# Kernel optimization log

Measured on AMD Instinct MI355X. Metric: run time of the kernel, lower is better.

Reference implementation:

```python
import jax, jax.numpy as jnp
import numpy as np

IN_CHANNELS = 192
BAND_DIM = IN_CHANNELS // 3   # 64
HEADS = 4
HEAD_DIM = BAND_DIM // HEADS  # 16
SCALE = HEAD_DIM ** -0.5


def setup_inputs() -> dict:
    key = jax.random.key(0)
    k1, k2, k3 = jax.random.split(key, 3)
    B, H, W = 8, 128, 128
    hf = jax.random.normal(k1, (B, IN_CHANNELS, H, W), dtype=jnp.float32)
    # torch Linear weights, stored as (in, out) for direct matmul
    W_qkv = jax.random.normal(k2, (BAND_DIM, 3 * BAND_DIM), dtype=jnp.float32) * (BAND_DIM ** -0.5)
    W_proj = jax.random.normal(k3, (BAND_DIM, BAND_DIM), dtype=jnp.float32) * (BAND_DIM ** -0.5)
    b_proj = jnp.zeros((BAND_DIM,), dtype=jnp.float32)
    res_scale = jnp.float32(0.5)
    return {"hf": hf, "W_qkv": W_qkv, "W_proj": W_proj, "b_proj": b_proj, "res_scale": res_scale}


def reference(hf, W_qkv, W_proj, b_proj, res_scale):
    B, Ctot, H, W = hf.shape
    bd, h, hd = BAND_DIM, HEADS, HEAD_DIM
    # (B, 3, bd, H, W) -> (B, H, W, 3, bd) -> (N, 3, bd)
    x = hf.reshape(B, 3, bd, H, W).transpose(0, 3, 4, 1, 2).reshape(-1, 3, bd)
    qkv = x @ W_qkv                                   # (N, 3, 3*bd)
    q, k, v = jnp.split(qkv, 3, axis=-1)
    # (N, 3, bd) -> (N, heads, 3, hd)
    def split_heads(t):
        return t.reshape(-1, 3, h, hd).transpose(0, 2, 1, 3)
    q, k, v = split_heads(q), split_heads(k), split_heads(v)
    attn = jnp.einsum('nhqd,nhkd->nhqk', q, k) * SCALE  # (N, heads, 3, 3)
    attn = jax.nn.softmax(attn, axis=-1)
    y = jnp.einsum('nhqk,nhkd->nhqd', attn, v)          # (N, heads, 3, hd)
    y = y.transpose(0, 2, 1, 3).reshape(-1, 3, bd)      # (N, 3, bd)
    y = y @ W_proj + b_proj
    # (N, 3, bd) -> (B, H, W, 3, bd) -> (B, Ctot, H, W)
    y = y.reshape(B, H, W, 3, bd).transpose(0, 3, 4, 1, 2).reshape(B, Ctot, H, W)
    return hf + res_scale * y
```

## Files before the change

kernel.cpp:

```cpp
#include <hip/hip_runtime.h>


typedef __attribute__((ext_vector_type(8))) short bf16x8;
typedef __attribute__((ext_vector_type(4))) float f32x4;

constexpr int kHW = 16384;
constexpr int kC = 192;

__device__ __forceinline__ unsigned short f2bf(float f) {
  unsigned int u = __float_as_uint(f);
  return (unsigned short)((u + 0x7fffu + ((u >> 16) & 1u)) >> 16);
}

__global__ void pack_weights(const float* __restrict__ Wqkv,
                             const float* __restrict__ Wproj,
                             unsigned char* __restrict__ wsc) {
  const int tid = threadIdx.x;
  const int wid = tid >> 6;
  const int l = tid & 63;
  const int c = l & 15;
  const int g = l >> 4;
  for (int f = wid; f < 24; f += 4) {
    const int m = f >> 1, s = f & 1;
    const int row = m * 16 + c;
    const int k0 = s * 32 + g * 8;
    bf16x8 wf;
#pragma unroll
    for (int j = 0; j < 8; ++j) wf[j] = (short)f2bf(Wqkv[(k0 + j) * 192 + row]);
    *(bf16x8*)(wsc + f * 1024 + l * 16) = wf;
  }
  for (int f = wid; f < 8; f += 4) {
    const int m = f >> 1, s = f & 1;
    const int row = m * 16 + c;
    const int k0 = s * 32 + g * 8;
    bf16x8 wf;
#pragma unroll
    for (int j = 0; j < 8; ++j) wf[j] = (short)f2bf(Wproj[(k0 + j) * 64 + row]);
    *(bf16x8*)(wsc + 24576 + f * 1024 + l * 16) = wf;
  }
}

template <int H>
__device__ __forceinline__ void head_compute(const char* wl, int l,
                                             const bf16x8 (&Xf)[3][2],
                                             uint2 (&pk)[3]) {
  const f32x4 zz = {0.f, 0.f, 0.f, 0.f};
  const bf16x8 qA0 = *(const bf16x8*)(wl + (H * 2 + 0) * 1024 + l * 16);
  const bf16x8 qA1 = *(const bf16x8*)(wl + (H * 2 + 1) * 1024 + l * 16);
  const bf16x8 kA0 = *(const bf16x8*)(wl + ((4 + H) * 2 + 0) * 1024 + l * 16);
  const bf16x8 kA1 = *(const bf16x8*)(wl + ((4 + H) * 2 + 1) * 1024 + l * 16);
  f32x4 q[3], k[3];
#pragma unroll
  for (int b = 0; b < 3; ++b) {
    q[b] = __builtin_amdgcn_mfma_f32_16x16x32_bf16(qA0, Xf[b][0], zz, 0, 0, 0);
    q[b] = __builtin_amdgcn_mfma_f32_16x16x32_bf16(qA1, Xf[b][1], q[b], 0, 0, 0);
    k[b] = __builtin_amdgcn_mfma_f32_16x16x32_bf16(kA0, Xf[b][0], zz, 0, 0, 0);
    k[b] = __builtin_amdgcn_mfma_f32_16x16x32_bf16(kA1, Xf[b][1], k[b], 0, 0, 0);
  }
  float P[3][3];
#pragma unroll
  for (int r1 = 0; r1 < 3; ++r1) {
    float sc[3];
#pragma unroll
    for (int r2 = 0; r2 < 3; ++r2) {
      float d = q[r1][0] * k[r2][0] + q[r1][1] * k[r2][1] +
                q[r1][2] * k[r2][2] + q[r1][3] * k[r2][3];
      d += __shfl_xor(d, 16);
      d += __shfl_xor(d, 32);
      sc[r2] = d * 0.25f;
    }
    const float mx = fmaxf(sc[0], fmaxf(sc[1], sc[2]));
    const float e0 = __expf(sc[0] - mx);
    const float e1 = __expf(sc[1] - mx);
    const float e2 = __expf(sc[2] - mx);
    const float inv = 1.f / (e0 + e1 + e2);
    P[r1][0] = e0 * inv;
    P[r1][1] = e1 * inv;
    P[r1][2] = e2 * inv;
  }
  const bf16x8 vA0 = *(const bf16x8*)(wl + ((8 + H) * 2 + 0) * 1024 + l * 16);
  const bf16x8 vA1 = *(const bf16x8*)(wl + ((8 + H) * 2 + 1) * 1024 + l * 16);
  f32x4 v[3];
#pragma unroll
  for (int b = 0; b < 3; ++b) {
    v[b] = __builtin_amdgcn_mfma_f32_16x16x32_bf16(vA0, Xf[b][0], zz, 0, 0, 0);
    v[b] = __builtin_amdgcn_mfma_f32_16x16x32_bf16(vA1, Xf[b][1], v[b], 0, 0, 0);
  }
#pragma unroll
  for (int r1 = 0; r1 < 3; ++r1) {
    f32x4 y = P[r1][0] * v[0] + P[r1][1] * v[1] + P[r1][2] * v[2];
    uint2 p;
    p.x = (unsigned)f2bf(y[0]) | ((unsigned)f2bf(y[1]) << 16);
    p.y = (unsigned)f2bf(y[2]) | ((unsigned)f2bf(y[3]) << 16);
    pk[r1] = p;
  }
}

__device__ __forceinline__ bf16x8 build_frag(uint2 pkA, uint2 pkB, int srcA,
                                             bool hi) {
  uint2 a0, a1, b0, b1;
  a0.x = (unsigned)__shfl((int)pkA.x, srcA, 64);
  a0.y = (unsigned)__shfl((int)pkA.y, srcA, 64);
  a1.x = (unsigned)__shfl((int)pkB.x, srcA, 64);
  a1.y = (unsigned)__shfl((int)pkB.y, srcA, 64);
  const int srcB = srcA + 16;
  b0.x = (unsigned)__shfl((int)pkA.x, srcB, 64);
  b0.y = (unsigned)__shfl((int)pkA.y, srcB, 64);
  b1.x = (unsigned)__shfl((int)pkB.x, srcB, 64);
  b1.y = (unsigned)__shfl((int)pkB.y, srcB, 64);
  const uint2 lo = hi ? a1 : a0;
  const uint2 hi2 = hi ? b1 : b0;
  union {
    unsigned u[4];
    bf16x8 v;
  } r;
  r.u[0] = lo.x;
  r.u[1] = lo.y;
  r.u[2] = hi2.x;
  r.u[3] = hi2.y;
  return r.v;
}

__global__ __launch_bounds__(256, 4) void hfattn_mfma10(
    const float* __restrict__ hf,
    const unsigned char* __restrict__ wfr,
    const float* __restrict__ bproj,
    const float* __restrict__ rscale,
    float* __restrict__ out) {
  __shared__ char wlds[32768];

  const int tid = threadIdx.x;
  const int wid = tid >> 6;
  const int l = tid & 63;
  const int c = l & 15;
  const int g = l >> 4;

  const f32x4 zz = {0.f, 0.f, 0.f, 0.f};

  const int pxB = blockIdx.x * 64 + wid * 16;
  const int b8 = pxB >> 14;
  const int blkBase = b8 * (kC * kHW);
  const int hw = (pxB & (kHW - 1)) + c;
  const float* __restrict__ hfp = hf + blkBase + hw;
  float* __restrict__ outp = out + blkBase + hw;

  const float rv = rscale[0];

#pragma unroll
  for (int i = 0; i < 8; ++i) {
    __builtin_amdgcn_global_load_lds(
        (const __attribute__((address_space(1))) unsigned int*)(wfr +
                                                                wid * 8192 +
                                                                i * 1024 +
                                                                l * 16),
        (__attribute__((address_space(3))) unsigned int*)(wlds + wid * 8192 +
                                                          i * 1024),
        16, 0, 0);
  }

  float xr[3][2][8];
#pragma unroll
  for (int b = 0; b < 3; ++b)
#pragma unroll
    for (int s = 0; s < 2; ++s)
#pragma unroll
      for (int j = 0; j < 8; ++j)
        xr[b][s][j] = hfp[(b * 64 + s * 32 + g * 8 + j) * kHW];
  __builtin_amdgcn_sched_barrier(0);

  bf16x8 Xf[3][2];
#pragma unroll
  for (int b = 0; b < 3; ++b)
#pragma unroll
    for (int s = 0; s < 2; ++s) {
      bf16x8 xf;
#pragma unroll
      for (int j = 0; j < 8; ++j) xf[j] = (short)f2bf(xr[b][s][j]);
      Xf[b][s] = xf;
    }

  asm volatile("s_waitcnt vmcnt(0)" ::: "memory");
  __syncthreads();

  const int srcA = ((g & 1) * 2) * 16 + c;
  const bool hi = (g >> 1) & 1;

  uint2 pkA[3], pkB[3];
  bf16x8 yS0[3], yS1[3];

  head_compute<0>(wlds, l, Xf, pkA);
  __builtin_amdgcn_sched_barrier(0);
  head_compute<1>(wlds, l, Xf, pkB);
  __builtin_amdgcn_sched_barrier(0);
#pragma unroll
  for (int b = 0; b < 3; ++b) yS0[b] = build_frag(pkA[b], pkB[b], srcA, hi);
  __builtin_amdgcn_sched_barrier(0);
  head_compute<2>(wlds, l, Xf, pkA);
  __builtin_amdgcn_sched_barrier(0);
  head_compute<3>(wlds, l, Xf, pkB);
  __builtin_amdgcn_sched_barrier(0);
#pragma unroll
  for (int b = 0; b < 3; ++b) yS1[b] = build_frag(pkA[b], pkB[b], srcA, hi);

  float bias_[4][4];
#pragma unroll
  for (int m = 0; m < 4; ++m) {
    const float4 bj = *(const float4*)(bproj + m * 16 + g * 4);
    bias_[m][0] = bj.x;
    bias_[m][1] = bj.y;
    bias_[m][2] = bj.z;
    bias_[m][3] = bj.w;
  }

#pragma unroll
  for (int b = 0; b < 3; ++b) {
#pragma unroll
    for (int m = 0; m < 4; ++m) {
      const bf16x8 pA0 =
          *(const bf16x8*)(wlds + (24 + m * 2 + 0) * 1024 + l * 16);
      const bf16x8 pA1 =
          *(const bf16x8*)(wlds + (24 + m * 2 + 1) * 1024 + l * 16);
      f32x4 o = __builtin_amdgcn_mfma_f32_16x16x32_bf16(pA0, yS0[b], zz, 0, 0, 0);
      o = __builtin_amdgcn_mfma_f32_16x16x32_bf16(pA1, yS1[b], o, 0, 0, 0);

      union {
        bf16x8 v;
        unsigned u[4];
      } su;
      su.v = Xf[b][m >> 1];
      const int hl = ((m & 1) * 2 + (g >> 1)) * 16 + c;
      const unsigned w0 = (unsigned)__shfl((int)su.u[0], hl, 64);
      const unsigned w1 = (unsigned)__shfl((int)su.u[1], hl, 64);
      const unsigned w2 = (unsigned)__shfl((int)su.u[2], hl, 64);
      const unsigned w3 = (unsigned)__shfl((int)su.u[3], hl, 64);
      const unsigned lo = (g & 1) ? w2 : w0;
      const unsigned hi2 = (g & 1) ? w3 : w1;
      float res[4];
      res[0] = __uint_as_float(lo << 16);
      res[1] = __uint_as_float(lo & 0xffff0000u);
      res[2] = __uint_as_float(hi2 << 16);
      res[3] = __uint_as_float(hi2 & 0xffff0000u);

#pragma unroll
      for (int j = 0; j < 4; ++j) {
        outp[(b * 64 + m * 16 + g * 4 + j) * kHW] =
            fmaf(rv, o[j] + bias_[m][j], res[j]);
      }
    }
  }
}

extern "C" void kernel_launch(void* const* d_in, const int* in_sizes, int n_in,
                              void* d_out, int out_size, void* d_ws,
                              size_t ws_size, hipStream_t stream) {
  const float* hf = (const float*)d_in[0];
  const float* Wqkv = (const float*)d_in[1];
  const float* Wproj = (const float*)d_in[2];
  const float* bproj = (const float*)d_in[3];
  const float* rscale = (const float*)d_in[4];
  float* out = (float*)d_out;
  unsigned char* wsc = (unsigned char*)d_ws;

  hipLaunchKernelGGL(pack_weights, dim3(1), dim3(256), 0, stream, Wqkv, Wproj,
                     wsc);

  const int npix = in_sizes[0] / kC;
  const int nblocks = npix / 64;
  hipLaunchKernelGGL(hfattn_mfma10, dim3(nblocks), dim3(256), 0, stream, hf,
                     wsc, bproj, rscale, out);
}
```

Before: 48.51 us.

## Process two pixel tiles per wave with software-pipelined input loads

Each wave now handles two 16-pixel tiles. The second tile's hf loads are issued before the first tile's attention compute, so global-memory latency overlaps MFMA work, and the LDS weight staging cost is amortized over twice as many pixels. The grid is halved and launch bounds drop to 3 blocks per SM to make room for the extra registers, which lowers occupancy. The bf16 conversion is also switched to the HIP library intrinsic.

```diff
diff --git a/kernel.cpp b/kernel.cpp
--- a/kernel.cpp
+++ b/kernel.cpp
@@ -1,4 +1,5 @@
 #include <hip/hip_runtime.h>
+#include <hip/hip_bf16.h>
 
 
 typedef __attribute__((ext_vector_type(8))) short bf16x8;
@@ -7,9 +8,8 @@
 constexpr int kHW = 16384;
 constexpr int kC = 192;
 
-__device__ __forceinline__ unsigned short f2bf(float f) {
-  unsigned int u = __float_as_uint(f);
-  return (unsigned short)((u + 0x7fffu + ((u >> 16) & 1u)) >> 16);
+__device__ __forceinline__ short f2bf(float f) {
+  return (short)__bfloat16_as_ushort(__float2bfloat16(f));
 }
 
 __global__ void pack_weights(const float* __restrict__ Wqkv,
@@ -26,7 +26,7 @@
     const int k0 = s * 32 + g * 8;
     bf16x8 wf;
 #pragma unroll
-    for (int j = 0; j < 8; ++j) wf[j] = (short)f2bf(Wqkv[(k0 + j) * 192 + row]);
+    for (int j = 0; j < 8; ++j) wf[j] = f2bf(Wqkv[(k0 + j) * 192 + row]);
     *(bf16x8*)(wsc + f * 1024 + l * 16) = wf;
   }
   for (int f = wid; f < 8; f += 4) {
@@ -35,7 +35,7 @@
     const int k0 = s * 32 + g * 8;
     bf16x8 wf;
 #pragma unroll
-    for (int j = 0; j < 8; ++j) wf[j] = (short)f2bf(Wproj[(k0 + j) * 64 + row]);
+    for (int j = 0; j < 8; ++j) wf[j] = f2bf(Wproj[(k0 + j) * 64 + row]);
     *(bf16x8*)(wsc + 24576 + f * 1024 + l * 16) = wf;
   }
 }
@@ -90,8 +90,10 @@
   for (int r1 = 0; r1 < 3; ++r1) {
     f32x4 y = P[r1][0] * v[0] + P[r1][1] * v[1] + P[r1][2] * v[2];
     uint2 p;
-    p.x = (unsigned)f2bf(y[0]) | ((unsigned)f2bf(y[1]) << 16);
-    p.y = (unsigned)f2bf(y[2]) | ((unsigned)f2bf(y[3]) << 16);
+    p.x = (unsigned)(unsigned short)f2bf(y[0]) |
+          ((unsigned)(unsigned short)f2bf(y[1]) << 16);
+    p.y = (unsigned)(unsigned short)f2bf(y[2]) |
+          ((unsigned)(unsigned short)f2bf(y[3]) << 16);
     pk[r1] = p;
   }
 }
@@ -121,44 +123,8 @@
   return r.v;
 }
 
-__global__ __launch_bounds__(256, 4) void hfattn_mfma10(
-    const float* __restrict__ hf,
-    const unsigned char* __restrict__ wfr,
-    const float* __restrict__ bproj,
-    const float* __restrict__ rscale,
-    float* __restrict__ out) {
-  __shared__ char wlds[32768];
-
-  const int tid = threadIdx.x;
-  const int wid = tid >> 6;
-  const int l = tid & 63;
-  const int c = l & 15;
-  const int g = l >> 4;
-
-  const f32x4 zz = {0.f, 0.f, 0.f, 0.f};
-
-  const int pxB = blockIdx.x * 64 + wid * 16;
-  const int b8 = pxB >> 14;
-  const int blkBase = b8 * (kC * kHW);
-  const int hw = (pxB & (kHW - 1)) + c;
-  const float* __restrict__ hfp = hf + blkBase + hw;
-  float* __restrict__ outp = out + blkBase + hw;
-
-  const float rv = rscale[0];
-
-#pragma unroll
-  for (int i = 0; i < 8; ++i) {
-    __builtin_amdgcn_global_load_lds(
-        (const __attribute__((address_space(1))) unsigned int*)(wfr +
-                                                                wid * 8192 +
-                                                                i * 1024 +
-                                                                l * 16),
-        (__attribute__((address_space(3))) unsigned int*)(wlds + wid * 8192 +
-                                                          i * 1024),
-        16, 0, 0);
-  }
-
-  float xr[3][2][8];
+__device__ __forceinline__ void loadX(const float* __restrict__ hfp, int g,
+                                      float (&xr)[3][2][8]) {
 #pragma unroll
   for (int b = 0; b < 3; ++b)
 #pragma unroll
@@ -166,28 +132,25 @@
 #pragma unroll
       for (int j = 0; j < 8; ++j)
         xr[b][s][j] = hfp[(b * 64 + s * 32 + g * 8 + j) * kHW];
-  __builtin_amdgcn_sched_barrier(0);
-
-  bf16x8 Xf[3][2];
+}
+
+__device__ __forceinline__ void convX(const float (&xr)[3][2][8],
+                                      bf16x8 (&Xf)[3][2]) {
 #pragma unroll
   for (int b = 0; b < 3; ++b)
 #pragma unroll
     for (int s = 0; s < 2; ++s) {
       bf16x8 xf;
 #pragma unroll
-      for (int j = 0; j < 8; ++j) xf[j] = (short)f2bf(xr[b][s][j]);
+      for (int j = 0; j < 8; ++j) xf[j] = f2bf(xr[b][s][j]);
       Xf[b][s] = xf;
     }
-
-  asm volatile("s_waitcnt vmcnt(0)" ::: "memory");
-  __syncthreads();
-
-  const int srcA = ((g & 1) * 2) * 16 + c;
-  const bool hi = (g >> 1) & 1;
-
+}
+
+__device__ __forceinline__ void tile_heads(const char* wlds, int l, int srcA,
+                                           bool hi, const bf16x8 (&Xf)[3][2],
+                                           bf16x8 (&yS0)[3], bf16x8 (&yS1)[3]) {
   uint2 pkA[3], pkB[3];
-  bf16x8 yS0[3], yS1[3];
-
   head_compute<0>(wlds, l, Xf, pkA);
   __builtin_amdgcn_sched_barrier(0);
   head_compute<1>(wlds, l, Xf, pkB);
@@ -201,17 +164,13 @@
   __builtin_amdgcn_sched_barrier(0);
 #pragma unroll
   for (int b = 0; b < 3; ++b) yS1[b] = build_frag(pkA[b], pkB[b], srcA, hi);
-
-  float bias_[4][4];
-#pragma unroll
-  for (int m = 0; m < 4; ++m) {
-    const float4 bj = *(const float4*)(bproj + m * 16 + g * 4);
-    bias_[m][0] = bj.x;
-    bias_[m][1] = bj.y;
-    bias_[m][2] = bj.z;
-    bias_[m][3] = bj.w;
-  }
-
+}
+
+__device__ __forceinline__ void tile_epilogue(
+    const char* wlds, int l, int g, int c, float rv, const float (&bias_)[4][4],
+    const bf16x8 (&Xf)[3][2], const bf16x8 (&yS0)[3], const bf16x8 (&yS1)[3],
+    float* __restrict__ outp) {
+  const f32x4 zz = {0.f, 0.f, 0.f, 0.f};
 #pragma unroll
   for (int b = 0; b < 3; ++b) {
 #pragma unroll
@@ -250,6 +209,83 @@
   }
 }
 
+__global__ __launch_bounds__(256, 3) void hfattn_mfma11(
+    const float* __restrict__ hf,
+    const unsigned char* __restrict__ wfr,
+    const float* __restrict__ bproj,
+    const float* __restrict__ rscale,
+    float* __restrict__ out) {
+  __shared__ char wlds[32768];
+
+  const int tid = threadIdx.x;
+  const int wid = tid >> 6;
+  const int l = tid & 63;
+  const int c = l & 15;
+  const int g = l >> 4;
+
+  const int pxB0 = blockIdx.x * 128 + wid * 32;
+  const int b8 = pxB0 >> 14;
+  const int blkBase = b8 * (kC * kHW);
+  const int hwA = (pxB0 & (kHW - 1)) + c;
+  const float* __restrict__ hfpA = hf + blkBase + hwA;
+  const float* __restrict__ hfpB = hfpA + 16;
+  float* __restrict__ outpA = out + blkBase + hwA;
+  float* __restrict__ outpB = outpA + 16;
+
+  const float rv = rscale[0];
+  const int srcA = ((g & 1) * 2) * 16 + c;
+  const bool hi = (g >> 1) & 1;
+
+#pragma unroll
+  for (int i = 0; i < 8; ++i) {
+    __builtin_amdgcn_global_load_lds(
+        (const __attribute__((address_space(1))) unsigned int*)(wfr +
+                                                                wid * 8192 +
+                                                                i * 1024 +
+                                                                l * 16),
+        (__attribute__((address_space(3))) unsigned int*)(wlds + wid * 8192 +
+                                                          i * 1024),
+        16, 0, 0);
+  }
+
+  float xrA[3][2][8];
+  loadX(hfpA, g, xrA);
+  __builtin_amdgcn_sched_barrier(0);
+  bf16x8 XfA[3][2];
+  convX(xrA, XfA);
+  asm volatile("s_waitcnt vmcnt(0)" ::: "memory");
+  __syncthreads();
+
+  float xrB[3][2][8];
+  loadX(hfpB, g, xrB);
+  __builtin_amdgcn_sched_barrier(0);
+
+  float bias_[4][4];
+#pragma unroll
+  for (int m = 0; m < 4; ++m) {
+    const float4 bj = *(const float4*)(bproj + m * 16 + g * 4);
+    bias_[m][0] = bj.x;
+    bias_[m][1] = bj.y;
+    bias_[m][2] = bj.z;
+    bias_[m][3] = bj.w;
+  }
+
+  bf16x8 yS0A[3], yS1A[3];
+  tile_heads(wlds, l, srcA, hi, XfA, yS0A, yS1A);
+  __builtin_amdgcn_sched_barrier(0);
+
+  bf16x8 XfB[3][2];
+  convX(xrB, XfB);
+  __builtin_amdgcn_sched_barrier(0);
+
+  tile_epilogue(wlds, l, g, c, rv, bias_, XfA, yS0A, yS1A, outpA);
+  __builtin_amdgcn_sched_barrier(0);
+
+  bf16x8 yS0B[3], yS1B[3];
+  tile_heads(wlds, l, srcA, hi, XfB, yS0B, yS1B);
+  tile_epilogue(wlds, l, g, c, rv, bias_, XfB, yS0B, yS1B, outpB);
+}
+
 extern "C" void kernel_launch(void* const* d_in, const int* in_sizes, int n_in,
                               void* d_out, int out_size, void* d_ws,
                               size_t ws_size, hipStream_t stream) {
@@ -265,7 +301,7 @@
                      wsc);
 
   const int npix = in_sizes[0] / kC;
-  const int nblocks = npix / 64;
-  hipLaunchKernelGGL(hfattn_mfma10, dim3(nblocks), dim3(256), 0, stream, hf,
+  const int nblocks = npix / 128;
+  hipLaunchKernelGGL(hfattn_mfma11, dim3(nblocks), dim3(256), 0, stream, hf,
                      wsc, bproj, rscale, out);
 }
```

Measured after the change: 81.04 us. +67.0%, slower.
